# Optimization experiments

Hardware: AMD Instinct MI355X
Metric: run time of the kernel (lower is better)

Reference implementation:

```python
import jax, jax.numpy as jnp
import numpy as np
from jax import lax

LAM = 1.0   # distance() calls wasserstein with lam=1
ITS = 20    # distance() calls wasserstein with its=20


def pdist2sq(X, Y):
    # squared Euclidean distance between all pairs: [nt,d],[nc,d] -> [nt,nc]
    return (-2.0 * (X @ Y.T)) + jnp.sum(Y * Y, axis=1)[None, :] + jnp.sum(X * X, axis=1)[:, None]


def setup_inputs() -> dict:
    key = jax.random.key(0)
    k1, k2 = jax.random.split(key)
    encoded = jax.random.normal(k1, (2048, 32, 256), dtype=jnp.float32)
    t = jax.random.randint(k2, (2048,), 0, 2, dtype=jnp.int32)
    return {"encoded": encoded, "seq_len": 32, "t": t}


def _wasserstein(encoded, t_np, seq_len):
    # t is an integer treatment indicator: constant w.r.t. the graph, so the
    # data-dependent split sizes are resolved on the host (like tf.where+gather).
    it = np.where(t_np > 0)[0]
    ic = np.where(t_np < 1)[0]
    nt, nc = int(it.shape[0]), int(ic.shape[0])
    p = float(t_np.mean())  # p_t = np.mean(t)

    Xt = jnp.transpose(encoded[it], (1, 0, 2))  # [S, nt, d]
    Xc = jnp.transpose(encoded[ic], (1, 0, 2))  # [S, nc, d]

    # marginal vectors (identical across timesteps)
    a = jnp.concatenate([(p / nt) * jnp.ones((nt, 1), jnp.float32),
                         (1.0 - p) * jnp.ones((1, 1), jnp.float32)], axis=0)  # [nt+1,1]
    b = jnp.concatenate([((1.0 - p) / nc) * jnp.ones((nc, 1), jnp.float32),
                         p * jnp.ones((1, 1), jnp.float32)], axis=0)          # [nc+1,1]

    def step(Xt_i, Xc_i):
        M = pdist2sq(Xt_i, Xc_i)                      # sq=True -> squared distances
        delta = lax.stop_gradient(jnp.max(M))
        eff_lam = lax.stop_gradient(LAM / jnp.mean(M))
        # pad with extra row/col of delta (zero in the corner)
        Mt = jnp.concatenate([M, delta * jnp.ones((1, nc), jnp.float32)], axis=0)
        col = jnp.concatenate([delta * jnp.ones((nt, 1), jnp.float32),
                               jnp.zeros((1, 1), jnp.float32)], axis=0)
        Mt = jnp.concatenate([Mt, col], axis=1)       # [nt+1, nc+1]
        K = jnp.exp(-eff_lam * Mt) + 1e-6
        ainvK = K / a

        def body(_, u):
            return 1.0 / (ainvK @ (b / (K.T @ u)))
        u = lax.fori_loop(0, ITS, body, a)            # Sinkhorn fixed point
        v = b / (K.T @ u)
        T = lax.stop_gradient(u * (v.T * K))          # backpropT=False
        return 2.0 * jnp.sum(T * Mt)

    return jnp.sum(jax.vmap(step)(Xt, Xc))


def reference(encoded, seq_len, t):
    t_np = np.asarray(t)
    return _wasserstein(encoded[:, :seq_len, :], t_np, seq_len)
```

## Files before the change

kernel.cpp:

```cpp
#include <hip/hip_runtime.h>
#include <hip/hip_bf16.h>

#define S_MAX  32
#define VST    2052
#define KSLOT  1057824
#define NCHUNK 16
#define YPST   2064

#define OFF_MAX  64
#define OFF_SUM  96
#define OFF_RNK  128
#define OFF_NORM 2176
#define OFF_U    67712
#define OFF_POOL 133376
#define OFF_YP   OFF_POOL
#define OFF_KF   8521984

typedef __attribute__((ext_vector_type(8))) short bf16x8;
typedef __attribute__((ext_vector_type(4))) float f32x4;

__device__ __forceinline__ float bflo(unsigned u) { return __uint_as_float(u << 16); }
__device__ __forceinline__ float bfhi(unsigned u) { return __uint_as_float(u & 0xffff0000u); }
__device__ __forceinline__ unsigned short f2bf(float f) {
    __hip_bfloat16 h = __float2bfloat16(f);
    return *reinterpret_cast<unsigned short*>(&h);
}

__global__ __launch_bounds__(1024) void idx_kernel(const int* __restrict__ t, float* __restrict__ ws) {
    __shared__ int sc[2048];
    const int tid = threadIdx.x;
    int p0 = (t[tid] > 0) ? 1 : 0;
    int p1 = (t[tid + 1024] > 0) ? 1 : 0;
    sc[tid] = p0; sc[tid + 1024] = p1;
    __syncthreads();
    for (int off = 1; off < 2048; off <<= 1) {
        int v0 = 0, v1 = 0;
        if (tid >= off)        v0 = sc[tid - off];
        if (tid + 1024 >= off) v1 = sc[tid + 1024 - off];
        __syncthreads();
        sc[tid] += v0; sc[tid + 1024] += v1;
        __syncthreads();
    }
    const int incl0 = sc[tid], incl1 = sc[tid + 1024];
    const int nt = sc[2047];
    const int nc = 2048 - nt;
    int* dst = (int*)(ws + OFF_RNK);
    dst[tid]        = p0 ? (incl0 - 1) : (2047 - (tid - incl0));
    dst[tid + 1024] = p1 ? (incl1 - 1) : (2047 - (tid + 1024 - incl1));
    if (tid == 0) {
        const float p = (float)nt / 2048.0f;
        ((int*)ws)[0] = nt;
        ((int*)ws)[1] = nc;
        ws[2] = p;
        ws[3] = p / (float)nt;
        ws[4] = 1.0f - p;
        ws[5] = (1.0f - p) / (float)nc;
        ws[6] = p;
    }
}

__global__ __launch_bounds__(256) void compact_kernel(const float* __restrict__ enc, float* __restrict__ ws) {
    const int gw = blockIdx.x * 4 + (threadIdx.x >> 6);
    const int lane = threadIdx.x & 63;
    const int n = gw >> 5, s = gw & 31;
    const int r = ((const int*)(ws + OFF_RNK))[n];
    const float4 v = *(const float4*)(enc + ((size_t)n * 32 + s) * 256 + lane * 4);
    float ss = v.x * v.x + v.y * v.y + v.z * v.z + v.w * v.w;
    for (int off = 32; off; off >>= 1) ss += __shfl_xor(ss, off);
    unsigned short* pool = reinterpret_cast<unsigned short*>(ws + OFF_POOL);
    ushort4 pk = { f2bf(v.x), f2bf(v.y), f2bf(v.z), f2bf(v.w) };
    *reinterpret_cast<ushort4*>(pool + ((size_t)(s * 2048 + r)) * 256 + lane * 4) = pk;
    if (lane == 0) ws[OFF_NORM + s * 2048 + r] = ss;
}

__global__ __launch_bounds__(256) void m_kernel(float* __restrict__ ws) {
    const int s = blockIdx.y;
    const int nt = ((const int*)ws)[0], nc = ((const int*)ws)[1];
    const int ldp = ((nc + 1) + 7) & ~7;
    const int nty = (nt + 127) >> 7, ncx = (nc + 127) >> 7;
    const int ntiles = nty * ncx;

    __shared__ float nrmA[128], nrmB[128];
    __shared__ float rmax[4], rsum[4];
    const int tid = threadIdx.x;
    const int lane = tid & 63, wave = tid >> 6;
    const int wr = wave >> 1, wc = wave & 1;
    const int row16 = lane & 15, koff = (lane >> 4) * 8;
    const unsigned short* pool = reinterpret_cast<const unsigned short*>(ws + OFF_POOL);
    const size_t sbase = (size_t)s * 2048 * 256;
    unsigned short* Ks = reinterpret_cast<unsigned short*>(ws + OFF_KF) + (size_t)s * KSLOT;

    float bmax = 0.0f, bsum = 0.0f;
    for (int tp = blockIdx.x; tp < ntiles; tp += 64) {
        const int by = tp / ncx, bx = tp - by * ncx;
        const int ibase = by * 128, jbase = bx * 128;

        __syncthreads();
        if (tid < 128) {
            nrmA[tid] = ws[OFF_NORM + s * 2048 + min(ibase + tid, 2047)];
        } else {
            const int j = jbase + (tid - 128);
            nrmB[tid - 128] = ws[OFF_NORM + s * 2048 + max(2047 - j, 0)];
        }
        __syncthreads();

        f32x4 acc[4][4] = {};
        #pragma unroll
        for (int d0 = 0; d0 < 256; d0 += 32) {
            bf16x8 af[4], bg[4];
            #pragma unroll
            for (int f = 0; f < 4; f++) {
                const int ar = min(ibase + wr * 64 + f * 16 + row16, 2047);
                const int br = max(2047 - (jbase + wc * 64 + f * 16 + row16), 0);
                af[f] = *(const bf16x8*)(pool + sbase + (size_t)ar * 256 + koff + d0);
                bg[f] = *(const bf16x8*)(pool + sbase + (size_t)br * 256 + koff + d0);
            }
            #pragma unroll
            for (int fi = 0; fi < 4; fi++)
                #pragma unroll
                for (int fj = 0; fj < 4; fj++)
                    acc[fi][fj] = __builtin_amdgcn_mfma_f32_16x16x32_bf16(af[fi], bg[fj], acc[fi][fj], 0, 0, 0);
        }

        const int crow = (lane >> 4) * 4, ccol = lane & 15;
        #pragma unroll
        for (int fi = 0; fi < 4; fi++) {
            #pragma unroll
            for (int fj = 0; fj < 4; fj++) {
                #pragma unroll
                for (int e = 0; e < 4; e++) {
                    const int ti = wr * 64 + fi * 16 + crow + e;
                    const int tj = wc * 64 + fj * 16 + ccol;
                    const int i = ibase + ti, j = jbase + tj;
                    if (i < nt && j < nc) {
                        float m = nrmA[ti] + nrmB[tj] - 2.0f * acc[fi][fj][e];
                        Ks[(size_t)i * ldp + j] = f2bf(m);
                        bmax = fmaxf(bmax, m);
                        bsum += m;
                    }
                }
            }
        }
    }
    for (int off = 32; off; off >>= 1) {
        bmax = fmaxf(bmax, __shfl_xor(bmax, off));
        bsum += __shfl_xor(bsum, off);
    }
    if (lane == 0) { rmax[wave] = bmax; rsum[wave] = bsum; }
    __syncthreads();
    if (tid == 0) {
        float bm = fmaxf(fmaxf(rmax[0], rmax[1]), fmaxf(rmax[2], rmax[3]));
        float bs = rsum[0] + rsum[1] + rsum[2] + rsum[3];
        atomicMax(&((unsigned int*)ws)[OFF_MAX + s], __float_as_uint(bm));
        atomicAdd(&ws[OFF_SUM + s], bs);
    }
}

__global__ __launch_bounds__(256) void phaseA0_kernel(float* __restrict__ ws) {
    const int s = blockIdx.y, chunk = blockIdx.x;
    const int nt = ((const int*)ws)[0], nc = ((const int*)ws)[1];
    const int R = nt + 1;
    const int ldp = ((nc + 1) + 7) & ~7;
    const int rpc = (R + NCHUNK - 1) / NCHUNK;
    const int r0 = chunk * rpc;
    const int rend = min(rpc, R - r0);
    const int j0 = threadIdx.x * 8;
    float* ypo = ws + OFF_YP + ((size_t)s * NCHUNK + chunk) * YPST;

    float acc[8];
    #pragma unroll
    for (int e = 0; e < 8; e++) acc[e] = 0.0f;

    if (j0 < ldp && rend > 0) {
        const float a_main = ws[3], a_last = ws[4];
        const float delta = __uint_as_float(((const unsigned int*)ws)[OFF_MAX + s]);
        const float lam = (float)nt * (float)nc / ws[OFF_SUM + s];
        const float kpad = __expf(-lam * delta) + 1e-6f;
        unsigned short* Kb = reinterpret_cast<unsigned short*>(ws + OFF_KF) + (size_t)s * KSLOT;

        #pragma unroll 2
        for (int r = 0; r < rend; r++) {
            const int i = r0 + r;
            unsigned short* Krow = Kb + (size_t)i * ldp + j0;
            uint4 kk = *reinterpret_cast<const uint4*>(Krow);
            float mv[8] = { bflo(kk.x), bfhi(kk.x), bflo(kk.y), bfhi(kk.y),
                            bflo(kk.z), bfhi(kk.z), bflo(kk.w), bfhi(kk.w) };
            const float uv = (i < nt) ? a_main : a_last;
            unsigned short pk[8];
            #pragma unroll
            for (int e = 0; e < 8; e++) {
                const int j = j0 + e;
                float kv;
                if (j > nc)       kv = 0.0f;
                else if (i == nt) kv = (j == nc) ? (1.0f + 1e-6f) : kpad;
                else if (j == nc) kv = kpad;
                else              kv = __expf(-lam * mv[e]) + 1e-6f;
                pk[e] = f2bf(kv);
                acc[e] += kv * uv;
            }
            uint4 st;
            st.x = (unsigned)pk[0] | ((unsigned)pk[1] << 16);
            st.y = (unsigned)pk[2] | ((unsigned)pk[3] << 16);
            st.z = (unsigned)pk[4] | ((unsigned)pk[5] << 16);
            st.w = (unsigned)pk[6] | ((unsigned)pk[7] << 16);
            *reinterpret_cast<uint4*>(Krow) = st;
        }
    }
    if (j0 < 2048) {
        float4 s0 = { acc[0], acc[1], acc[2], acc[3] };
        float4 s1 = { acc[4], acc[5], acc[6], acc[7] };
        *reinterpret_cast<float4*>(ypo + j0)     = s0;
        *reinterpret_cast<float4*>(ypo + j0 + 4) = s1;
    }
}

__global__ __launch_bounds__(256) void fusedBA_kernel(float* __restrict__ ws, int par) {
    const int s = blockIdx.y, chunk = blockIdx.x;
    const int nt = ((const int*)ws)[0], nc = ((const int*)ws)[1];
    const int R = nt + 1;
    const int ldp = ((nc + 1) + 7) & ~7;
    const int rpc = (R + NCHUNK - 1) / NCHUNK;
    const int r0 = chunk * rpc;
    const int rend = min(rpc, R - r0);
    const int tid = threadIdx.x, lane = tid & 63, wave = tid >> 6;
    const float a_main = ws[3], a_last = ws[4];
    const float b_main = ws[5], b_last = ws[6];

    __shared__ __align__(16) float w_l[2056];
    __shared__ __align__(16) float ldsm[4][2056];

    for (int j = tid; j < 4 * 2056; j += 256) (&ldsm[0][0])[j] = 0.0f;

    {
        const float* yp = ws + OFF_YP + ((size_t)par * S_MAX + s) * (NCHUNK * YPST);
        for (int j0 = tid * 4; j0 < 2056; j0 += 1024) {
            float4 wv = {0.f, 0.f, 0.f, 0.f};
            if (j0 <= nc) {
                float4 sum = {0.f, 0.f, 0.f, 0.f};
                #pragma unroll
                for (int c = 0; c < NCHUNK; c++) {
                    float4 v = *reinterpret_cast<const float4*>(yp + (size_t)c * YPST + j0);
                    sum.x += v.x; sum.y += v.y; sum.z += v.z; sum.w += v.w;
                }
                wv.x = (j0 + 0 <= nc) ? (((j0 + 0 < nc) ? b_main : b_last) / sum.x) : 0.f;
                wv.y = (j0 + 1 <= nc) ? (((j0 + 1 < nc) ? b_main : b_last) / sum.y) : 0.f;
                wv.z = (j0 + 2 <= nc) ? (((j0 + 2 < nc) ? b_main : b_last) / sum.z) : 0.f;
                wv.w = (j0 + 3 <= nc) ? (((j0 + 3 < nc) ? b_main : b_last) / sum.w) : 0.f;
            }
            *reinterpret_cast<float4*>(&w_l[j0]) = wv;
        }
    }
    __syncthreads();

    const unsigned short* Kb = reinterpret_cast<const unsigned short*>(ws + OFF_KF) + (size_t)s * KSLOT;
    float* u = ws + OFF_U + s * VST;

    float va[4][8];
    #pragma unroll
    for (int t = 0; t < 4; t++)
        #pragma unroll
        for (int e = 0; e < 8; e++) va[t][e] = 0.0f;

    for (int base = wave * 2; base < rend; base += 8) {
        const int i0 = r0 + base;
        const bool two = (base + 1 < rend);
        const int i1 = two ? (i0 + 1) : i0;
        const unsigned short* Kr0 = Kb + (size_t)i0 * ldp;
        const unsigned short* Kr1 = Kb + (size_t)i1 * ldp;

        float kf0[4][8], kf1[4][8];
        float d0 = 0.0f, d1 = 0.0f;
        #pragma unroll
        for (int t = 0; t < 4; t++) {
            const int j8 = lane * 8 + t * 512;
            if (t * 512 < ldp) {
                uint4 k0 = {0u,0u,0u,0u}, k1 = {0u,0u,0u,0u};
                if (j8 < ldp) {
                    k0 = *reinterpret_cast<const uint4*>(Kr0 + j8);
                    k1 = *reinterpret_cast<const uint4*>(Kr1 + j8);
                }
                kf0[t][0] = bflo(k0.x); kf0[t][1] = bfhi(k0.x);
                kf0[t][2] = bflo(k0.y); kf0[t][3] = bfhi(k0.y);
                kf0[t][4] = bflo(k0.z); kf0[t][5] = bfhi(k0.z);
                kf0[t][6] = bflo(k0.w); kf0[t][7] = bfhi(k0.w);
                kf1[t][0] = bflo(k1.x); kf1[t][1] = bfhi(k1.x);
                kf1[t][2] = bflo(k1.y); kf1[t][3] = bfhi(k1.y);
                kf1[t][4] = bflo(k1.z); kf1[t][5] = bfhi(k1.z);
                kf1[t][6] = bflo(k1.w); kf1[t][7] = bfhi(k1.w);
                const float* wp = &w_l[j8];
                #pragma unroll
                for (int e = 0; e < 8; e++) {
                    d0 += kf0[t][e] * wp[e];
                    d1 += kf1[t][e] * wp[e];
                }
            } else {
                #pragma unroll
                for (int e = 0; e < 8; e++) { kf0[t][e] = 0.f; kf1[t][e] = 0.f; }
            }
        }
        for (int off = 32; off; off >>= 1) {
            d0 += __shfl_xor(d0, off);
            d1 += __shfl_xor(d1, off);
        }
        const float u0 = ((i0 < nt) ? a_main : a_last) / d0;
        const float u1 = ((i1 < nt) ? a_main : a_last) / d1;
        if (lane == 0) {
            u[i0] = u0;
            if (two) u[i1] = u1;
        }
        const float u1e = two ? u1 : 0.0f;
        #pragma unroll
        for (int t = 0; t < 4; t++)
            #pragma unroll
            for (int e = 0; e < 8; e++)
                va[t][e] += kf0[t][e] * u0 + kf1[t][e] * u1e;
    }

    #pragma unroll
    for (int t = 0; t < 4; t++) {
        if (t * 512 < ldp) {
            const int j8 = lane * 8 + t * 512;
            if (j8 < ldp) {
                float4 v0 = { va[t][0], va[t][1], va[t][2], va[t][3] };
                float4 v1 = { va[t][4], va[t][5], va[t][6], va[t][7] };
                *reinterpret_cast<float4*>(&ldsm[wave][j8])     = v0;
                *reinterpret_cast<float4*>(&ldsm[wave][j8 + 4]) = v1;
            }
        }
    }
    __syncthreads();

    float* ypo = ws + OFF_YP + (((size_t)(par ^ 1) * S_MAX + s) * NCHUNK + chunk) * YPST;
    for (int j0 = tid * 4; j0 < 2056; j0 += 1024) {
        float4 a0 = *reinterpret_cast<const float4*>(&ldsm[0][j0]);
        float4 a1 = *reinterpret_cast<const float4*>(&ldsm[1][j0]);
        float4 a2 = *reinterpret_cast<const float4*>(&ldsm[2][j0]);
        float4 a3 = *reinterpret_cast<const float4*>(&ldsm[3][j0]);
        float4 r;
        r.x = (a0.x + a1.x) + (a2.x + a3.x);
        r.y = (a0.y + a1.y) + (a2.y + a3.y);
        r.z = (a0.z + a1.z) + (a2.z + a3.z);
        r.w = (a0.w + a1.w) + (a2.w + a3.w);
        *reinterpret_cast<float4*>(ypo + j0) = r;
    }
}

__global__ __launch_bounds__(256) void value_kernel(float* __restrict__ ws, const int* __restrict__ seqlen,
                                                    float* __restrict__ out) {
    const int s = blockIdx.y, chunk = blockIdx.x;
    const int nt = ((const int*)ws)[0], nc = ((const int*)ws)[1];
    const int R = nt + 1;
    const int ldp = ((nc + 1) + 7) & ~7;
    const int rpc = (R + NCHUNK - 1) / NCHUNK;
    const int r0 = chunk * rpc;
    const int rend = min(rpc, R - r0);
    const float b_main = ws[5], b_last = ws[6];
    const float meanM = ws[OFF_SUM + s] / ((float)nt * (float)nc);
    const float* u = ws + OFF_U + s * VST;
    const int tid = threadIdx.x, lane = tid & 63, wave = tid >> 6;

    __shared__ __align__(16) float w_l[2056];
    __shared__ float wred[4];
    {
        const float* yp = ws + OFF_YP + (size_t)s * (NCHUNK * YPST);
        for (int j0 = tid * 4; j0 < 2056; j0 += 1024) {
            float4 wv = {0.f, 0.f, 0.f, 0.f};
            if (j0 <= nc) {
                float4 sum = {0.f, 0.f, 0.f, 0.f};
                #pragma unroll
                for (int c = 0; c < NCHUNK; c++) {
                    float4 v = *reinterpret_cast<const float4*>(yp + (size_t)c * YPST + j0);
                    sum.x += v.x; sum.y += v.y; sum.z += v.z; sum.w += v.w;
                }
                wv.x = (j0 + 0 <= nc) ? (((j0 + 0 < nc) ? b_main : b_last) / sum.x) : 0.f;
                wv.y = (j0 + 1 <= nc) ? (((j0 + 1 < nc) ? b_main : b_last) / sum.y) : 0.f;
                wv.z = (j0 + 2 <= nc) ? (((j0 + 2 < nc) ? b_main : b_last) / sum.z) : 0.f;
                wv.w = (j0 + 3 <= nc) ? (((j0 + 3 < nc) ? b_main : b_last) / sum.w) : 0.f;
            }
            *reinterpret_cast<float4*>(&w_l[j0]) = wv;
        }
    }
    __syncthreads();

    const unsigned short* Kb = reinterpret_cast<const unsigned short*>(ws + OFF_KF) + (size_t)s * KSLOT;
    float wsum = 0.0f;
    for (int rr = wave; rr < rend; rr += 4) {
        const int i = r0 + rr;
        const unsigned short* Krow = Kb + (size_t)i * ldp;
        float acc = 0.0f;
        for (int j8 = lane * 8; j8 < ldp; j8 += 512) {
            uint4 kk = *reinterpret_cast<const uint4*>(Krow + j8);
            float4 w0 = *reinterpret_cast<const float4*>(&w_l[j8]);
            float4 w1 = *reinterpret_cast<const float4*>(&w_l[j8 + 4]);
            float k0 = bflo(kk.x), k1 = bfhi(kk.x), k2 = bflo(kk.y), k3 = bfhi(kk.y);
            float k4 = bflo(kk.z), k5 = bfhi(kk.z), k6 = bflo(kk.w), k7 = bfhi(kk.w);
            acc += k0 * (-__logf(fmaxf(k0 - 1e-6f, 1e-30f))) * w0.x
                 + k1 * (-__logf(fmaxf(k1 - 1e-6f, 1e-30f))) * w0.y
                 + k2 * (-__logf(fmaxf(k2 - 1e-6f, 1e-30f))) * w0.z
                 + k3 * (-__logf(fmaxf(k3 - 1e-6f, 1e-30f))) * w0.w
                 + k4 * (-__logf(fmaxf(k4 - 1e-6f, 1e-30f))) * w1.x
                 + k5 * (-__logf(fmaxf(k5 - 1e-6f, 1e-30f))) * w1.y
                 + k6 * (-__logf(fmaxf(k6 - 1e-6f, 1e-30f))) * w1.z
                 + k7 * (-__logf(fmaxf(k7 - 1e-6f, 1e-30f))) * w1.w;
        }
        acc *= meanM;
        for (int off = 32; off; off >>= 1) acc += __shfl_xor(acc, off);
        wsum += u[i] * acc;
    }
    if (lane == 0) wred[wave] = wsum;
    __syncthreads();
    if (tid == 0 && s < *seqlen)
        atomicAdd(out, 2.0f * (wred[0] + wred[1] + wred[2] + wred[3]));
}

extern "C" void kernel_launch(void* const* d_in, const int* in_sizes, int n_in,
                              void* d_out, int out_size, void* d_ws, size_t ws_size,
                              hipStream_t stream) {
    const float* enc  = (const float*)d_in[0];
    const int* seqlen = (const int*)d_in[1];
    const int* t      = (const int*)d_in[2];
    float* out = (float*)d_out;
    float* ws  = (float*)d_ws;

    hipMemsetAsync(d_out, 0, sizeof(float), stream);
    hipMemsetAsync(d_ws, 0, 128 * sizeof(float), stream);

    idx_kernel    <<<1, 1024, 0, stream>>>(t, ws);
    compact_kernel<<<16384, 256, 0, stream>>>(enc, ws);
    m_kernel      <<<dim3(64, 32), 256, 0, stream>>>(ws);

    const dim3 pg(NCHUNK, 32);
    phaseA0_kernel<<<pg, 256, 0, stream>>>(ws);
    for (int k = 0; k < 20; k++)
        fusedBA_kernel<<<pg, 256, 0, stream>>>(ws, k & 1);
    value_kernel  <<<pg, 256, 0, stream>>>(ws, seqlen, out);
}
```

Before: 770.3 us.

## Stage GEMM tiles in LDS and process four Sinkhorn rows per wave

Measured after the change: 747.2 us. 3.0% less time.

```diff
diff --git a/kernel.cpp b/kernel.cpp
--- a/kernel.cpp
+++ b/kernel.cpp
@@ -80,6 +80,8 @@
     const int nty = (nt + 127) >> 7, ncx = (nc + 127) >> 7;
     const int ntiles = nty * ncx;
 
+    __shared__ unsigned short As[128][72];
+    __shared__ unsigned short Bs[128][72];
     __shared__ float nrmA[128], nrmB[128];
     __shared__ float rmax[4], rsum[4];
     const int tid = threadIdx.x;
@@ -90,6 +92,8 @@
     const size_t sbase = (size_t)s * 2048 * 256;
     unsigned short* Ks = reinterpret_cast<unsigned short*>(ws + OFF_KF) + (size_t)s * KSLOT;
 
+    const int srow = tid >> 3, scg = (tid & 7) * 8;
+
     float bmax = 0.0f, bsum = 0.0f;
     for (int tp = blockIdx.x; tp < ntiles; tp += 64) {
         const int by = tp / ncx, bx = tp - by * ncx;
@@ -102,24 +106,36 @@
             const int j = jbase + (tid - 128);
             nrmB[tid - 128] = ws[OFF_NORM + s * 2048 + max(2047 - j, 0)];
         }
-        __syncthreads();
 
         f32x4 acc[4][4] = {};
         #pragma unroll
-        for (int d0 = 0; d0 < 256; d0 += 32) {
-            bf16x8 af[4], bg[4];
-            #pragma unroll
-            for (int f = 0; f < 4; f++) {
-                const int ar = min(ibase + wr * 64 + f * 16 + row16, 2047);
-                const int br = max(2047 - (jbase + wc * 64 + f * 16 + row16), 0);
-                af[f] = *(const bf16x8*)(pool + sbase + (size_t)ar * 256 + koff + d0);
-                bg[f] = *(const bf16x8*)(pool + sbase + (size_t)br * 256 + koff + d0);
-            }
-            #pragma unroll
-            for (int fi = 0; fi < 4; fi++)
-                #pragma unroll
-                for (int fj = 0; fj < 4; fj++)
-                    acc[fi][fj] = __builtin_amdgcn_mfma_f32_16x16x32_bf16(af[fi], bg[fj], acc[fi][fj], 0, 0, 0);
+        for (int d0 = 0; d0 < 256; d0 += 64) {
+            __syncthreads();
+            #pragma unroll
+            for (int it = 0; it < 4; it++) {
+                const int row = it * 32 + srow;
+                const int ar = min(ibase + row, 2047);
+                const int br = max(2047 - (jbase + row), 0);
+                *reinterpret_cast<uint4*>(&As[row][scg]) =
+                    *reinterpret_cast<const uint4*>(pool + sbase + (size_t)ar * 256 + d0 + scg);
+                *reinterpret_cast<uint4*>(&Bs[row][scg]) =
+                    *reinterpret_cast<const uint4*>(pool + sbase + (size_t)br * 256 + d0 + scg);
+            }
+            __syncthreads();
+            #pragma unroll
+            for (int ks = 0; ks < 2; ks++) {
+                bf16x8 af[4], bg[4];
+                #pragma unroll
+                for (int f = 0; f < 4; f++) {
+                    af[f] = *reinterpret_cast<const bf16x8*>(&As[wr * 64 + f * 16 + row16][ks * 32 + koff]);
+                    bg[f] = *reinterpret_cast<const bf16x8*>(&Bs[wc * 64 + f * 16 + row16][ks * 32 + koff]);
+                }
+                #pragma unroll
+                for (int fi = 0; fi < 4; fi++)
+                    #pragma unroll
+                    for (int fj = 0; fj < 4; fj++)
+                        acc[fi][fj] = __builtin_amdgcn_mfma_f32_16x16x32_bf16(af[fi], bg[fj], acc[fi][fj], 0, 0, 0);
+            }
         }
 
         const int crow = (lane >> 4) * 4, ccol = lane & 15;
@@ -261,71 +277,73 @@
         #pragma unroll
         for (int e = 0; e < 8; e++) va[t][e] = 0.0f;
 
-    for (int base = wave * 2; base < rend; base += 8) {
-        const int i0 = r0 + base;
-        const bool two = (base + 1 < rend);
-        const int i1 = two ? (i0 + 1) : i0;
-        const unsigned short* Kr0 = Kb + (size_t)i0 * ldp;
-        const unsigned short* Kr1 = Kb + (size_t)i1 * ldp;
-
-        float kf0[4][8], kf1[4][8];
-        float d0 = 0.0f, d1 = 0.0f;
+    for (int base = wave * 4; base < rend; base += 16) {
+        int ii[4]; bool act[4];
+        const unsigned short* Kr[4];
+        #pragma unroll
+        for (int r = 0; r < 4; r++) {
+            act[r] = (base + r) < rend;
+            ii[r] = r0 + (act[r] ? (base + r) : base);
+            Kr[r] = Kb + (size_t)ii[r] * ldp;
+        }
+        float kf[4][4][8];
+        float d[4] = {0.f, 0.f, 0.f, 0.f};
         #pragma unroll
         for (int t = 0; t < 4; t++) {
             const int j8 = lane * 8 + t * 512;
             if (t * 512 < ldp) {
-                uint4 k0 = {0u,0u,0u,0u}, k1 = {0u,0u,0u,0u};
-                if (j8 < ldp) {
-                    k0 = *reinterpret_cast<const uint4*>(Kr0 + j8);
-                    k1 = *reinterpret_cast<const uint4*>(Kr1 + j8);
-                }
-                kf0[t][0] = bflo(k0.x); kf0[t][1] = bfhi(k0.x);
-                kf0[t][2] = bflo(k0.y); kf0[t][3] = bfhi(k0.y);
-                kf0[t][4] = bflo(k0.z); kf0[t][5] = bfhi(k0.z);
-                kf0[t][6] = bflo(k0.w); kf0[t][7] = bfhi(k0.w);
-                kf1[t][0] = bflo(k1.x); kf1[t][1] = bfhi(k1.x);
-                kf1[t][2] = bflo(k1.y); kf1[t][3] = bfhi(k1.y);
-                kf1[t][4] = bflo(k1.z); kf1[t][5] = bfhi(k1.z);
-                kf1[t][6] = bflo(k1.w); kf1[t][7] = bfhi(k1.w);
-                const float* wp = &w_l[j8];
-                #pragma unroll
-                for (int e = 0; e < 8; e++) {
-                    d0 += kf0[t][e] * wp[e];
-                    d1 += kf1[t][e] * wp[e];
+                const bool in = (j8 < ldp);
+                float wreg[8];
+                #pragma unroll
+                for (int e = 0; e < 8; e++) wreg[e] = in ? w_l[j8 + e] : 0.0f;
+                #pragma unroll
+                for (int r = 0; r < 4; r++) {
+                    uint4 kk = {0u, 0u, 0u, 0u};
+                    if (in) kk = *reinterpret_cast<const uint4*>(Kr[r] + j8);
+                    kf[r][t][0] = bflo(kk.x); kf[r][t][1] = bfhi(kk.x);
+                    kf[r][t][2] = bflo(kk.y); kf[r][t][3] = bfhi(kk.y);
+                    kf[r][t][4] = bflo(kk.z); kf[r][t][5] = bfhi(kk.z);
+                    kf[r][t][6] = bflo(kk.w); kf[r][t][7] = bfhi(kk.w);
+                    #pragma unroll
+                    for (int e = 0; e < 8; e++) d[r] += kf[r][t][e] * wreg[e];
                 }
             } else {
                 #pragma unroll
-                for (int e = 0; e < 8; e++) { kf0[t][e] = 0.f; kf1[t][e] = 0.f; }
+                for (int r = 0; r < 4; r++)
+                    #pragma unroll
+                    for (int e = 0; e < 8; e++) kf[r][t][e] = 0.0f;
             }
         }
         for (int off = 32; off; off >>= 1) {
-            d0 += __shfl_xor(d0, off);
-            d1 += __shfl_xor(d1, off);
-        }
-        const float u0 = ((i0 < nt) ? a_main : a_last) / d0;
-        const float u1 = ((i1 < nt) ? a_main : a_last) / d1;
+            d[0] += __shfl_xor(d[0], off);
+            d[1] += __shfl_xor(d[1], off);
+            d[2] += __shfl_xor(d[2], off);
+            d[3] += __shfl_xor(d[3], off);
+        }
+        float uu[4];
+        #pragma unroll
+        for (int r = 0; r < 4; r++)
+            uu[r] = act[r] ? (((ii[r] < nt) ? a_main : a_last) / d[r]) : 0.0f;
         if (lane == 0) {
-            u[i0] = u0;
-            if (two) u[i1] = u1;
-        }
-        const float u1e = two ? u1 : 0.0f;
+            #pragma unroll
+            for (int r = 0; r < 4; r++) if (act[r]) u[ii[r]] = uu[r];
+        }
         #pragma unroll
         for (int t = 0; t < 4; t++)
             #pragma unroll
             for (int e = 0; e < 8; e++)
-                va[t][e] += kf0[t][e] * u0 + kf1[t][e] * u1e;
+                va[t][e] += kf[0][t][e] * uu[0] + kf[1][t][e] * uu[1]
+                          + kf[2][t][e] * uu[2] + kf[3][t][e] * uu[3];
     }
 
     #pragma unroll
     for (int t = 0; t < 4; t++) {
-        if (t * 512 < ldp) {
-            const int j8 = lane * 8 + t * 512;
-            if (j8 < ldp) {
-                float4 v0 = { va[t][0], va[t][1], va[t][2], va[t][3] };
-                float4 v1 = { va[t][4], va[t][5], va[t][6], va[t][7] };
-                *reinterpret_cast<float4*>(&ldsm[wave][j8])     = v0;
-                *reinterpret_cast<float4*>(&ldsm[wave][j8 + 4]) = v1;
-            }
+        const int j8 = lane * 8 + t * 512;
+        if (t * 512 < ldp && j8 < ldp) {
+            float4 v0 = { va[t][0], va[t][1], va[t][2], va[t][3] };
+            float4 v1 = { va[t][4], va[t][5], va[t][6], va[t][7] };
+            *reinterpret_cast<float4*>(&ldsm[wave][j8])     = v0;
+            *reinterpret_cast<float4*>(&ldsm[wave][j8 + 4]) = v1;
         }
     }
     __syncthreads();
```
